# Performance work log

Measured on AMD Instinct MI355X. Metric: run time of the kernel, lower is better.

The kernel has to match this reference:

```python
import jax, jax.numpy as jnp
import numpy as np

N, T, U, D, V = 8, 200, 100, 512, 500


def setup_inputs() -> dict:
    key = jax.random.key(0)
    k1, k2, k3, k4 = jax.random.split(key, 4)
    encoder_out = jax.random.normal(k1, (N, T, D), dtype=jnp.float32)
    decoder_out = jax.random.normal(k2, (N, U, D), dtype=jnp.float32)
    # nn.Linear(input_dim, output_dim): weight (V, D), bias (V,)
    bound = 1.0 / np.sqrt(D)
    W = jax.random.uniform(k3, (V, D), minval=-bound, maxval=bound, dtype=jnp.float32)
    b = jax.random.uniform(k4, (V,), minval=-bound, maxval=bound, dtype=jnp.float32)
    return {"encoder_out": encoder_out, "decoder_out": decoder_out, "W": W, "b": b}


def reference(encoder_out, decoder_out, W, b):
    # broadcast add: (N,T,1,D) + (N,1,U,D) -> (N,T,U,D)
    x = encoder_out[:, :, None, :] + decoder_out[:, None, :, :]
    activations = jnp.tanh(x)
    # linear: (N,T,U,D) @ (D,V) + b -> (N,T,U,V)
    logits = jnp.einsum("ntud,vd->ntuv", activations, W) + b
    return logits
```

## Files before the change

### kernel.cpp

```cpp
#include <hip/hip_runtime.h>
#include <hip/hip_bf16.h>


#define NB 8
#define TT 200
#define UU 100
#define DD 512
#define VV 500
#define VP 512
#define BM 64
#define BNB 256
#define BK 32
#define KSTEPS 16
#define THREADS 256
#define LDA 40
#define LCH 264
#define MROWS (NB*TT*UU)
#define MBLOCKS (MROWS/BM)

typedef __attribute__((ext_vector_type(4))) float         f32x4;
typedef __attribute__((ext_vector_type(8))) short         s16x8;
typedef __attribute__((ext_vector_type(4))) unsigned int  u32x4;

__device__ __forceinline__ unsigned short f2bf(float f) {
    unsigned int u = __builtin_bit_cast(unsigned int, f);
    u = (u + 0x7FFFu + ((u >> 16) & 1u)) >> 16;
    return (unsigned short)u;
}

__device__ __forceinline__ unsigned int cvt_pk_bf16(float a, float b) {
    unsigned int r;
    asm("v_cvt_pk_bf16_f32 %0, %1, %2" : "=v"(r) : "v"(a), "v"(b));
    return r;
}

__device__ __forceinline__ float fast_tanh(float x) {
    float e = __builtin_amdgcn_exp2f(x * 2.88539008177793f);
    return __builtin_fmaf(-2.0f, __builtin_amdgcn_rcpf(e + 1.0f), 1.0f);
}

__global__ void prep_w(const float* __restrict__ W, unsigned short* __restrict__ Wt) {
    int idx = blockIdx.x * 256 + threadIdx.x;
    int k = idx & 511;
    int v = idx >> 9;
    float val = (v < VV) ? W[v * DD + k] : 0.0f;
    Wt[(k >> 5) * (VP * BK) + v * BK + (k & 31)] = f2bf(val);
}

#define KBODY(kc, CUR, NXT, BC, BNX)                                          \
  {                                                                           \
    if ((kc) < KSTEPS - 1) {                                                  \
      _Pragma("unroll")                                                       \
      for (int f = 0; f < 4; ++f)                                             \
        BNX[f] = *(const s16x8*)(wptr + ((kc)+1) * (VP * BK) + f * (16*BK));  \
      const float* e2 = ep + ((kc)+1) * BK;                                   \
      const float* d2 = dp + ((kc)+1) * BK;                                   \
      e0 = *(const f32x4*)(e2);  e1 = *(const f32x4*)(e2 + 4);                \
      d0 = *(const f32x4*)(d2);  d1 = *(const f32x4*)(d2 + 4);                \
    }                                                                         \
    s16x8 aF[4];                                                              \
    _Pragma("unroll")                                                         \
    for (int m = 0; m < 4; ++m)                                               \
      aF[m] = *(const s16x8*)(&CUR[(m * 16 + lr) * LDA + lk * 8]);            \
    __builtin_amdgcn_s_setprio(1);                                            \
    _Pragma("unroll")                                                         \
    for (int m = 0; m < 4; ++m)                                               \
      _Pragma("unroll")                                                       \
      for (int f = 0; f < 4; ++f)                                             \
        acc[m][f] = __builtin_amdgcn_mfma_f32_16x16x32_bf16(aF[m], BC[f],     \
                                                            acc[m][f],0,0,0); \
    __builtin_amdgcn_s_setprio(0);                                            \
    if ((kc) < KSTEPS - 1) {                                                  \
      u32x4 wds;                                                              \
      wds[0] = cvt_pk_bf16(fast_tanh(e0[0]+d0[0]), fast_tanh(e0[1]+d0[1]));   \
      wds[1] = cvt_pk_bf16(fast_tanh(e0[2]+d0[2]), fast_tanh(e0[3]+d0[3]));   \
      wds[2] = cvt_pk_bf16(fast_tanh(e1[0]+d1[0]), fast_tanh(e1[1]+d1[1]));   \
      wds[3] = cvt_pk_bf16(fast_tanh(e1[2]+d1[2]), fast_tanh(e1[3]+d1[3]));   \
      *(u32x4*)(&NXT[srow * LDA + sk]) = wds;                                 \
    }                                                                         \
    __syncthreads();                                                          \
  }

__global__ __launch_bounds__(THREADS, 3) void joiner_kernel(
    const float* __restrict__ enc, const float* __restrict__ dec,
    const unsigned short* __restrict__ Wt, const float* __restrict__ bias,
    float* __restrict__ out)
{
    __shared__ __align__(16) char smem[16 * LCH * 4];
    unsigned short* lA0 = (unsigned short*)smem;
    unsigned short* lA1 = (unsigned short*)(smem + BM * LDA * 2);

    const int tid  = threadIdx.x;
    const int mb   = blockIdx.x;
    const int vb   = blockIdx.y;
    const int lane = tid & 63;
    const int wn   = tid >> 6;
    const int lr   = lane & 15;
    const int lk   = lane >> 4;

    const int srow = tid >> 2;
    const int sk   = (tid & 3) << 3;

    int r   = mb * BM + srow;
    int n   = r / (TT * UU);
    int rem = r - n * (TT * UU);
    int t   = rem / UU;
    int u   = rem - t * UU;
    const float* ep = enc + (n * TT + t) * DD + sk;
    const float* dp = dec + (n * UU + u) * DD + sk;

    const unsigned short* wptr = Wt + (vb * BNB + wn * 64 + lr) * BK + lk * 8;

    f32x4 e0, e1, d0, d1;
    s16x8 b0[4], b1[4];

    e0 = *(const f32x4*)(ep);     e1 = *(const f32x4*)(ep + 4);
    d0 = *(const f32x4*)(dp);     d1 = *(const f32x4*)(dp + 4);
    #pragma unroll
    for (int f = 0; f < 4; ++f)
        b0[f] = *(const s16x8*)(wptr + f * (16 * BK));
    {
        u32x4 wds;
        wds[0] = cvt_pk_bf16(fast_tanh(e0[0]+d0[0]), fast_tanh(e0[1]+d0[1]));
        wds[1] = cvt_pk_bf16(fast_tanh(e0[2]+d0[2]), fast_tanh(e0[3]+d0[3]));
        wds[2] = cvt_pk_bf16(fast_tanh(e1[0]+d1[0]), fast_tanh(e1[1]+d1[1]));
        wds[3] = cvt_pk_bf16(fast_tanh(e1[2]+d1[2]), fast_tanh(e1[3]+d1[3]));
        *(u32x4*)(&lA0[srow * LDA + sk]) = wds;
    }
    __syncthreads();

    f32x4 acc[4][4];
    #pragma unroll
    for (int m = 0; m < 4; ++m)
        #pragma unroll
        for (int f = 0; f < 4; ++f)
            acc[m][f] = (f32x4){0.f, 0.f, 0.f, 0.f};

    #pragma unroll
    for (int kk = 0; kk < KSTEPS; kk += 2) {
        KBODY(kk,     lA0, lA1, b0, b1)
        KBODY(kk + 1, lA1, lA0, b1, b0)
    }

    float bv[4];
    #pragma unroll
    for (int f = 0; f < 4; ++f) {
        int v = vb * BNB + wn * 64 + f * 16 + lr;
        bv[f] = (v < VV) ? bias[v] : 0.0f;
    }

    float* lchunk = (float*)smem;
    const int slabcols = (vb == 0) ? BNB : (VV - BNB);
    const int segmax   = slabcols >> 2;
    float* outbase = out + (long)mb * BM * VV + vb * BNB;

    for (int c = 0; c < 4; ++c) {
        __syncthreads();
        #pragma unroll
        for (int f = 0; f < 4; ++f) {
            int vloc = wn * 64 + f * 16 + lr;
            #pragma unroll
            for (int q = 0; q < 4; ++q)
                lchunk[(lk * 4 + q) * LCH + vloc] = acc[c][f][q] + bv[f];
        }
        __syncthreads();
        float* dst = outbase + c * 16 * VV;
        #pragma unroll
        for (int i = 0; i < 4; ++i) {
            int idx = i * THREADS + tid;
            int row = idx >> 6;
            int seg = idx & 63;
            if (seg < segmax)
                *(f32x4*)(dst + row * VV + seg * 4) =
                    *(const f32x4*)(lchunk + row * LCH + seg * 4);
        }
    }
}

extern "C" void kernel_launch(void* const* d_in, const int* in_sizes, int n_in,
                              void* d_out, int out_size, void* d_ws, size_t ws_size,
                              hipStream_t stream) {
    const float* enc = (const float*)d_in[0];
    const float* dec = (const float*)d_in[1];
    const float* W   = (const float*)d_in[2];
    const float* b   = (const float*)d_in[3];
    float* out = (float*)d_out;
    unsigned short* Wt = (unsigned short*)d_ws;

    prep_w<<<dim3((VP * DD) / 256), dim3(256), 0, stream>>>(W, Wt);
    joiner_kernel<<<dim3(MBLOCKS, 2), dim3(THREADS), 0, stream>>>(enc, dec, Wt, b, out);
}
```

Baseline: 154.0 us.

## Cover full vocab per block and restructure K-loop prefetch and barriers

```diff
diff --git a/kernel.cpp b/kernel.cpp
--- a/kernel.cpp
+++ b/kernel.cpp
@@ -9,12 +9,10 @@
 #define VV 500
 #define VP 512
 #define BM 64
-#define BNB 256
 #define BK 32
 #define KSTEPS 16
 #define THREADS 256
 #define LDA 40
-#define LCH 264
 #define MROWS (NB*TT*UU)
 #define MBLOCKS (MROWS/BM)
 
@@ -49,27 +47,18 @@
 
 #define KBODY(kc, CUR, NXT, BC, BNX)                                          \
   {                                                                           \
+       \
     if ((kc) < KSTEPS - 1) {                                                  \
       _Pragma("unroll")                                                       \
-      for (int f = 0; f < 4; ++f)                                             \
+      for (int f = 0; f < 8; ++f)                                             \
         BNX[f] = *(const s16x8*)(wptr + ((kc)+1) * (VP * BK) + f * (16*BK));  \
-      const float* e2 = ep + ((kc)+1) * BK;                                   \
-      const float* d2 = dp + ((kc)+1) * BK;                                   \
-      e0 = *(const f32x4*)(e2);  e1 = *(const f32x4*)(e2 + 4);                \
-      d0 = *(const f32x4*)(d2);  d1 = *(const f32x4*)(d2 + 4);                \
     }                                                                         \
+                                               \
     s16x8 aF[4];                                                              \
     _Pragma("unroll")                                                         \
     for (int m = 0; m < 4; ++m)                                               \
       aF[m] = *(const s16x8*)(&CUR[(m * 16 + lr) * LDA + lk * 8]);            \
-    __builtin_amdgcn_s_setprio(1);                                            \
-    _Pragma("unroll")                                                         \
-    for (int m = 0; m < 4; ++m)                                               \
-      _Pragma("unroll")                                                       \
-      for (int f = 0; f < 4; ++f)                                             \
-        acc[m][f] = __builtin_amdgcn_mfma_f32_16x16x32_bf16(aF[m], BC[f],     \
-                                                            acc[m][f],0,0,0); \
-    __builtin_amdgcn_s_setprio(0);                                            \
+                     \
     if ((kc) < KSTEPS - 1) {                                                  \
       u32x4 wds;                                                              \
       wds[0] = cvt_pk_bf16(fast_tanh(e0[0]+d0[0]), fast_tanh(e0[1]+d0[1]));   \
@@ -77,22 +66,40 @@
       wds[2] = cvt_pk_bf16(fast_tanh(e1[0]+d1[0]), fast_tanh(e1[1]+d1[1]));   \
       wds[3] = cvt_pk_bf16(fast_tanh(e1[2]+d1[2]), fast_tanh(e1[3]+d1[3]));   \
       *(u32x4*)(&NXT[srow * LDA + sk]) = wds;                                 \
+      if ((kc) < KSTEPS - 2) {                                                \
+        const float* e2 = ep + ((kc)+2) * BK;                                 \
+        const float* d2 = dp + ((kc)+2) * BK;                                 \
+        e0 = *(const f32x4*)(e2);  e1 = *(const f32x4*)(e2 + 4);              \
+        d0 = *(const f32x4*)(d2);  d1 = *(const f32x4*)(d2 + 4);              \
+      }                                                                       \
     }                                                                         \
-    __syncthreads();                                                          \
+                    \
+    __builtin_amdgcn_s_setprio(1);                                            \
+    _Pragma("unroll")                                                         \
+    for (int m = 0; m < 4; ++m)                                               \
+      _Pragma("unroll")                                                       \
+      for (int f = 0; f < 8; ++f)                                             \
+        acc[m][f] = __builtin_amdgcn_mfma_f32_16x16x32_bf16(aF[m], BC[f],     \
+                                                            acc[m][f],0,0,0); \
+    __builtin_amdgcn_s_setprio(0);                                            \
+                \
+    if ((kc) < KSTEPS - 1) {                                                  \
+      asm volatile("s_waitcnt lgkmcnt(0)" ::: "memory");                      \
+      __builtin_amdgcn_s_barrier();                                           \
+    }                                                                         \
   }
 
-__global__ __launch_bounds__(THREADS, 3) void joiner_kernel(
+__global__ __launch_bounds__(THREADS, 2) void joiner_kernel(
     const float* __restrict__ enc, const float* __restrict__ dec,
     const unsigned short* __restrict__ Wt, const float* __restrict__ bias,
     float* __restrict__ out)
 {
-    __shared__ __align__(16) char smem[16 * LCH * 4];
+    __shared__ __align__(16) char smem[32000];
     unsigned short* lA0 = (unsigned short*)smem;
     unsigned short* lA1 = (unsigned short*)(smem + BM * LDA * 2);
 
     const int tid  = threadIdx.x;
     const int mb   = blockIdx.x;
-    const int vb   = blockIdx.y;
     const int lane = tid & 63;
     const int wn   = tid >> 6;
     const int lr   = lane & 15;
@@ -109,15 +116,15 @@
     const float* ep = enc + (n * TT + t) * DD + sk;
     const float* dp = dec + (n * UU + u) * DD + sk;
 
-    const unsigned short* wptr = Wt + (vb * BNB + wn * 64 + lr) * BK + lk * 8;
+    const unsigned short* wptr = Wt + (wn * 128 + lr) * BK + lk * 8;
 
     f32x4 e0, e1, d0, d1;
-    s16x8 b0[4], b1[4];
+    s16x8 b0[8], b1[8];
 
     e0 = *(const f32x4*)(ep);     e1 = *(const f32x4*)(ep + 4);
     d0 = *(const f32x4*)(dp);     d1 = *(const f32x4*)(dp + 4);
     #pragma unroll
-    for (int f = 0; f < 4; ++f)
+    for (int f = 0; f < 8; ++f)
         b0[f] = *(const s16x8*)(wptr + f * (16 * BK));
     {
         u32x4 wds;
@@ -127,13 +134,16 @@
         wds[3] = cvt_pk_bf16(fast_tanh(e1[2]+d1[2]), fast_tanh(e1[3]+d1[3]));
         *(u32x4*)(&lA0[srow * LDA + sk]) = wds;
     }
-    __syncthreads();
+    e0 = *(const f32x4*)(ep + BK);     e1 = *(const f32x4*)(ep + BK + 4);
+    d0 = *(const f32x4*)(dp + BK);     d1 = *(const f32x4*)(dp + BK + 4);
+    asm volatile("s_waitcnt lgkmcnt(0)" ::: "memory");
+    __builtin_amdgcn_s_barrier();
 
-    f32x4 acc[4][4];
+    f32x4 acc[4][8];
     #pragma unroll
     for (int m = 0; m < 4; ++m)
         #pragma unroll
-        for (int f = 0; f < 4; ++f)
+        for (int f = 0; f < 8; ++f)
             acc[m][f] = (f32x4){0.f, 0.f, 0.f, 0.f};
 
     #pragma unroll
@@ -142,37 +152,34 @@
         KBODY(kk + 1, lA1, lA0, b1, b0)
     }
 
-    float bv[4];
+    float bv[8];
     #pragma unroll
-    for (int f = 0; f < 4; ++f) {
-        int v = vb * BNB + wn * 64 + f * 16 + lr;
+    for (int f = 0; f < 8; ++f) {
+        int v = wn * 128 + f * 16 + lr;
         bv[f] = (v < VV) ? bias[v] : 0.0f;
     }
 
     float* lchunk = (float*)smem;
-    const int slabcols = (vb == 0) ? BNB : (VV - BNB);
-    const int segmax   = slabcols >> 2;
-    float* outbase = out + (long)mb * BM * VV + vb * BNB;
+    float* outbase = out + (long)mb * BM * VV;
 
-    for (int c = 0; c < 4; ++c) {
+    for (int m = 0; m < 4; ++m) {
         __syncthreads();
         #pragma unroll
-        for (int f = 0; f < 4; ++f) {
-            int vloc = wn * 64 + f * 16 + lr;
-            #pragma unroll
-            for (int q = 0; q < 4; ++q)
-                lchunk[(lk * 4 + q) * LCH + vloc] = acc[c][f][q] + bv[f];
+        for (int f = 0; f < 8; ++f) {
+            int v = wn * 128 + f * 16 + lr;
+            if (v < VV) {
+                #pragma unroll
+                for (int q = 0; q < 4; ++q)
+                    lchunk[(lk * 4 + q) * VV + v] = acc[m][f][q] + bv[f];
+            }
         }
         __syncthreads();
-        float* dst = outbase + c * 16 * VV;
+        float* dst = outbase + m * 16 * VV;
         #pragma unroll
-        for (int i = 0; i < 4; ++i) {
-            int idx = i * THREADS + tid;
-            int row = idx >> 6;
-            int seg = idx & 63;
-            if (seg < segmax)
-                *(f32x4*)(dst + row * VV + seg * 4) =
-                    *(const f32x4*)(lchunk + row * LCH + seg * 4);
+        for (int i = 0; i < 8; ++i) {
+            int c = i * THREADS + tid;
+            if (c < 2000)
+                *(f32x4*)(dst + c * 4) = *(const f32x4*)(lchunk + c * 4);
         }
     }
 }
@@ -188,5 +195,5 @@
     unsigned short* Wt = (unsigned short*)d_ws;
 
     prep_w<<<dim3((VP * DD) / 256), dim3(256), 0, stream>>>(W, Wt);
-    joiner_kernel<<<dim3(MBLOCKS, 2), dim3(THREADS), 0, stream>>>(enc, dec, Wt, b, out);
+    joiner_kernel<<<dim3(MBLOCKS), dim3(THREADS), 0, stream>>>(enc, dec, Wt, b, out);
 }
```

Measured after the change: 130.6 us. 15.2% less time.
